# Kernel optimization log

Measured on AMD Instinct MI355X. Metric: run time of the kernel, lower is better.

The kernel has to match this reference:

```python
import jax, jax.numpy as jnp
import numpy as np

B, S, H, HKV, D = 2, 1024, 32, 8, 128


def _rope_tables(seq_len, head_dim, base=10000.0):
    inv_freq = 1.0 / (base ** (np.arange(0, head_dim, 2, dtype=np.float32) / head_dim))
    freqs = np.arange(seq_len, dtype=np.float32)[:, None] * inv_freq[None, :]  # [S, D/2]
    emb = np.concatenate([freqs, freqs], axis=-1)  # [S, D] (Llama layout)
    return jnp.asarray(np.cos(emb)), jnp.asarray(np.sin(emb))


def setup_inputs() -> dict:
    key = jax.random.key(0)
    kq, kk, kv = jax.random.split(key, 3)
    q = jax.random.normal(kq, (B, S, H, D), dtype=jnp.float32)
    k = jax.random.normal(kk, (B, S, HKV, D), dtype=jnp.float32)
    v = jax.random.normal(kv, (B, S, HKV, D), dtype=jnp.float32)
    cos, sin = _rope_tables(S, D)
    # additive causal mask [B, 1, S, S]: 0 where allowed, large negative where masked
    causal = jnp.tril(jnp.ones((S, S), dtype=bool))
    mask = jnp.where(causal, 0.0, -1e9).astype(jnp.float32)
    attention_mask = jnp.broadcast_to(mask[None, None], (B, 1, S, S))
    softmax_scale = 1.0 / float(np.sqrt(D))
    return {
        "query_states": q, "key_states": k, "value_states": v,
        "cos": cos, "sin": sin, "attention_mask": attention_mask,
        "softmax_scale": softmax_scale,
    }


def _apply_rope(x, cos, sin):
    # x: [B, S, h, D]; cos/sin: [S, D]
    d2 = x.shape[-1] // 2
    rot = jnp.concatenate([-x[..., d2:], x[..., :d2]], axis=-1)  # rotate_half
    return x * cos[None, :, None, :] + rot * sin[None, :, None, :]


def reference(query_states, key_states, value_states, cos, sin, attention_mask, softmax_scale):
    b, s, h, d = query_states.shape
    hkv = key_states.shape[2]
    g = h // hkv  # GQA group size
    q = _apply_rope(query_states, cos, sin)
    k = _apply_rope(key_states, cos, sin)
    qg = q.reshape(b, s, hkv, g, d)
    # scores: [B, Hkv, G, Q, K]
    scores = jnp.einsum('bqhgd,bkhd->bhgqk', qg, k) * softmax_scale
    scores = scores + attention_mask[:, :, None]  # [B,1,Q,K] -> broadcast over (Hkv, G)
    p = jax.nn.softmax(scores, axis=-1)
    out = jnp.einsum('bhgqk,bkhd->bqhgd', p, value_states)
    return out.reshape(b, s, h, d)
```

## Files before the change

kernel.cpp:

```cpp
#include <hip/hip_runtime.h>

#define S_LEN 1024
#define D_DIM 128
#define NH    32
#define NKV   8
#define NB    2

typedef __bf16 bf16x8 __attribute__((ext_vector_type(8)));
typedef float  f32x4  __attribute__((ext_vector_type(4)));
typedef unsigned short u16x8 __attribute__((ext_vector_type(8)));

__device__ __forceinline__ unsigned short f2bf(float f) {
    unsigned int u = __float_as_uint(f);
    u += 0x7fffu + ((u >> 16) & 1u);
    return (unsigned short)(u >> 16);
}

__device__ __forceinline__ void gld_lds16(const unsigned short* g, unsigned short* l) {
    __builtin_amdgcn_global_load_lds(
        (const __attribute__((address_space(1))) unsigned int*)(g),
        (__attribute__((address_space(3))) unsigned int*)(l), 16, 0, 0);
}

__global__ __launch_bounds__(256) void prep_kernel(
    const float* __restrict__ q, const float* __restrict__ k,
    const float* __restrict__ v, const float* __restrict__ cosb,
    const float* __restrict__ sinb, const float* __restrict__ scale_ptr,
    unsigned short* __restrict__ Qr, unsigned short* __restrict__ Kr,
    unsigned short* __restrict__ Vt)
{
    const int bx  = blockIdx.x;
    const int tid = threadIdx.x;
    __shared__ __align__(16) unsigned short tile[64][132];
    if (bx < 16384) {
        const float sc = *scale_ptr * 1.44269504088896f;
        int gid = bx * 256 + tid;
        int row = gid >> 6;
        int j   = gid & 63;
        int h  = row & (NH - 1);
        int bs = row >> 5;
        int s  = bs & (S_LEN - 1);
        int b  = bs >> 10;
        const float* qp = q + (size_t)row * D_DIM;
        float x0 = qp[j];
        float x1 = qp[j + 64];
        float c  = cosb[s * D_DIM + j];
        float sn = sinb[s * D_DIM + j];
        size_t orow = ((size_t)(b * NH + h) * S_LEN + s) * D_DIM;
        Qr[orow + j]      = f2bf((x0 * c - x1 * sn) * sc);
        Qr[orow + j + 64] = f2bf((x1 * c + x0 * sn) * sc);
    } else if (bx < 20480) {
        int gid = (bx - 16384) * 256 + tid;
        int row = gid >> 6;
        int j   = gid & 63;
        int hk = row & (NKV - 1);
        int bs = row >> 3;
        int s  = bs & (S_LEN - 1);
        int b  = bs >> 10;
        const float* kp = k + (size_t)row * D_DIM;
        float x0 = kp[j];
        float x1 = kp[j + 64];
        float c  = cosb[s * D_DIM + j];
        float sn = sinb[s * D_DIM + j];
        size_t orow = ((size_t)(b * NKV + hk) * S_LEN + s) * D_DIM;
        Kr[orow + j]      = f2bf(x0 * c - x1 * sn);
        Kr[orow + j + 64] = f2bf(x1 * c + x0 * sn);
    } else {
        int blk   = bx - 20480;
        int stile = blk & 15;
        int hk    = (blk >> 4) & (NKV - 1);
        int b     = blk >> 7;
#pragma unroll
        for (int i = 0; i < 8; i++) {
            int e    = i * 256 + tid;
            int srow = e >> 5;
            int dq   = (e & 31) * 4;
            const float* vp = v + (((size_t)(b * S_LEN + stile * 64 + srow) * NKV + hk) * D_DIM + dq);
            float4 val = *(const float4*)vp;
            tile[srow][dq + 0] = f2bf(val.x);
            tile[srow][dq + 1] = f2bf(val.y);
            tile[srow][dq + 2] = f2bf(val.z);
            tile[srow][dq + 3] = f2bf(val.w);
        }
        __syncthreads();
        size_t head = (size_t)(b * NKV + hk) * D_DIM * S_LEN;
#pragma unroll
        for (int i = 0; i < 4; i++) {
            int g  = i * 256 + tid;
            int d  = g >> 3;
            int c8 = g & 7;
            int s0 = c8 * 8;
            u16x8 pk;
#pragma unroll
            for (int jj = 0; jj < 8; jj++) pk[jj] = tile[s0 + jj][d];
            *(u16x8*)(Vt + head + (size_t)d * S_LEN + stile * 64 + s0) = pk;
        }
    }
}

__global__ __launch_bounds__(256) void attn_kernel(
    const unsigned short* __restrict__ Qr,
    const unsigned short* __restrict__ Kr,
    const unsigned short* __restrict__ Vt,
    float* __restrict__ out)
{
    const int bid = blockIdx.x;
    const int g   = bid >> 8;
    const int m   = (bid >> 6) & 3;
    const int qt  = (g == 0) ? (15 - m) : (g == 1) ? (8 + m)
                  : (g == 2) ? (7 - m)  : m;
    const int head = bid & 63;
    const int h    = head & 31;
    const int b    = head >> 5;
    const int hk   = h >> 2;

    const int tid  = threadIdx.x;
    const int w    = tid >> 6;
    const int lane = tid & 63;
    const int lr   = lane & 15;
    const int lg   = lane >> 4;

    __shared__ __align__(16) unsigned short Kt[2][32 * 128];
    __shared__ __align__(16) unsigned short Vs[2][128 * 32];
    __shared__ __align__(16) unsigned short Pb[4][16 * 32];

    const int qw = qt * 64 + w * 16;
    const int U  = 2 * qt + 2;

    const unsigned short* khead = Kr + (size_t)(b * NKV + hk) * S_LEN * D_DIM;
    const unsigned short* vhead = Vt + (size_t)(b * NKV + hk) * D_DIM * S_LEN;

    const int krow = lane >> 4;
    const int kcc  = lane & 15;
    const int vrw  = lane >> 2;
    const int vcc  = lane & 3;

    auto stage = [&](int u, int buf) {
        const unsigned short* kt = khead + (size_t)u * 32 * D_DIM;
#pragma unroll
        for (int n = 0; n < 2; n++) {
            int row = w * 8 + n * 4 + krow;
            int cc  = kcc ^ (row & 7);
            gld_lds16(kt + (size_t)row * D_DIM + cc * 8, &Kt[buf][(w * 8 + n * 4) * 128]);
        }
        const unsigned short* vt = vhead + (size_t)u * 32;
#pragma unroll
        for (int n = 0; n < 2; n++) {
            int d  = w * 32 + n * 16 + vrw;
            int cc = vcc ^ (d & 3);
            gld_lds16(vt + (size_t)d * S_LEN + cc * 8, &Vs[buf][(w * 32 + n * 16) * 32]);
        }
    };

    const unsigned short* qbase =
        Qr + ((size_t)(b * NH + h) * S_LEN + qw + lr) * D_DIM;
    bf16x8 qf[4];
#pragma unroll
    for (int kk = 0; kk < 4; kk++)
        qf[kk] = *(const bf16x8*)(qbase + lg * 8 + kk * 32);

    f32x4 o[8];
#pragma unroll
    for (int dt = 0; dt < 8; dt++) o[dt] = f32x4{0.f, 0.f, 0.f, 0.f};
    float m_run = -1e30f, lsum = 0.f;

    stage(0, 0);

#pragma unroll 1
    for (int u = 0; u < U; ++u) {
        const int cur = u & 1;
        __syncthreads();
        if (u + 1 < U) stage(u + 1, cur ^ 1);

        if (32 * u <= qw + 15) {
            const bool act1 = (32 * u + 16 <= qw + 15);

            f32x4 st[2];
            st[0] = f32x4{0.f, 0.f, 0.f, 0.f};
            st[1] = f32x4{0.f, 0.f, 0.f, 0.f};
            __builtin_amdgcn_s_setprio(1);
#pragma unroll
            for (int kj = 0; kj < 2; kj++) {
                if (kj == 0 || act1) {
                    int row = kj * 16 + lr;
#pragma unroll
                    for (int kk = 0; kk < 4; kk++) {
                        int cs = (lg + kk * 4) ^ (row & 7);
                        bf16x8 kf = *(const bf16x8*)(&Kt[cur][row * 128 + cs * 8]);
                        st[kj] = __builtin_amdgcn_mfma_f32_16x16x32_bf16(kf, qf[kk], st[kj], 0, 0, 0);
                    }
                }
            }
            __builtin_amdgcn_s_setprio(0);

            if (32 * u + 31 > qw) {
#pragma unroll
                for (int kj = 0; kj < 2; kj++)
#pragma unroll
                    for (int r = 0; r < 4; r++)
                        if (32 * u + kj * 16 + lg * 4 + r > qw + lr) st[kj][r] = -1e30f;
            }

            float mx = fmaxf(fmaxf(st[0][0], st[0][1]), fmaxf(st[0][2], st[0][3]));
            mx = fmaxf(mx, fmaxf(fmaxf(st[1][0], st[1][1]), fmaxf(st[1][2], st[1][3])));
            float pm = fmaxf(mx, __shfl_xor(mx, 16));
            pm = fmaxf(pm, __shfl_xor(pm, 32));

            if (__any(pm > m_run + 8.f)) {
                float mnew = fmaxf(m_run, pm);
                float ps   = exp2f(m_run - mnew);
                m_run = mnew;
                lsum *= ps;
#pragma unroll
                for (int r = 0; r < 4; r++) {
                    float psr = __shfl(ps, lg * 4 + r);
#pragma unroll
                    for (int dt = 0; dt < 8; dt++) o[dt][r] *= psr;
                }
            }
            float ls = 0.f;
#pragma unroll
            for (int kj = 0; kj < 2; kj++)
#pragma unroll
                for (int r = 0; r < 4; r++) {
                    float p = exp2f(st[kj][r] - m_run);
                    st[kj][r] = p;
                    ls += p;
                }
            float t = ls + __shfl_xor(ls, 16);
            t += __shfl_xor(t, 32);
            lsum += t;

            char* pw = (char*)&Pb[w][0];
#pragma unroll
            for (int kj = 0; kj < 2; kj++) {
                unsigned int w0 = (unsigned)f2bf(st[kj][0]) | ((unsigned)f2bf(st[kj][1]) << 16);
                unsigned int w1 = (unsigned)f2bf(st[kj][2]) | ((unsigned)f2bf(st[kj][3]) << 16);
                int C = (2 * kj + (lg >> 1)) ^ (lr & 3);
                *(uint2*)(pw + lr * 64 + C * 16 + (lg & 1) * 8) = uint2{w0, w1};
            }

            __builtin_amdgcn_s_setprio(1);
            int Cp = lg ^ (lr & 3);
            bf16x8 pf = *(const bf16x8*)(pw + lr * 64 + Cp * 16);
#pragma unroll
            for (int dt = 0; dt < 8; dt++) {
                int vrow = dt * 16 + lr;
                int cs2 = lg ^ (vrow & 3);
                bf16x8 vf = *(const bf16x8*)(&Vs[cur][vrow * 32 + cs2 * 8]);
                o[dt] = __builtin_amdgcn_mfma_f32_16x16x32_bf16(pf, vf, o[dt], 0, 0, 0);
            }
            __builtin_amdgcn_s_setprio(0);
        }
    }

    float rcp = 1.0f / lsum;
    float invr[4];
#pragma unroll
    for (int r = 0; r < 4; r++) invr[r] = __shfl(rcp, lg * 4 + r);
    float* obase = out + ((size_t)(b * S_LEN + qw) * NH + h) * D_DIM;
#pragma unroll
    for (int dt = 0; dt < 8; dt++)
#pragma unroll
        for (int r = 0; r < 4; r++)
            obase[(size_t)(lg * 4 + r) * NH * D_DIM + dt * 16 + lr] = o[dt][r] * invr[r];
}

extern "C" void kernel_launch(void* const* d_in, const int* in_sizes, int n_in,
                              void* d_out, int out_size, void* d_ws, size_t ws_size,
                              hipStream_t stream) {
    const float* q    = (const float*)d_in[0];
    const float* k    = (const float*)d_in[1];
    const float* v    = (const float*)d_in[2];
    const float* cosb = (const float*)d_in[3];
    const float* sinb = (const float*)d_in[4];
    const float* scale = (const float*)d_in[6];
    float* out = (float*)d_out;

    unsigned short* Qr = (unsigned short*)d_ws;
    unsigned short* Kr = Qr + (size_t)NB * NH  * S_LEN * D_DIM;
    unsigned short* Vt = Kr + (size_t)NB * NKV * S_LEN * D_DIM;

    prep_kernel<<<20736, 256, 0, stream>>>(q, k, v, cosb, sinb, scale, Qr, Kr, Vt);
    attn_kernel<<<1024, 256, 0, stream>>>(Qr, Kr, Vt, out);
}
```

Before: 73.45 us.

## Use 64-key tiles, pair causal query tiles per block, keep P in registers

The attention kernel now stages 64-key K/V tiles instead of 32 and launches 512 blocks. Each block handles two query tiles (15-p and p) in sequence, which balances causal work across blocks. The softmax probabilities are packed straight into MFMA A-operand registers, and the V fragments are gathered with split 8-byte LDS reads, so the per-wave P round trip through shared memory is gone. The costs are doubled LDS footprint, fewer blocks in flight, more registers, and a sync between the two passes.

```diff
diff --git a/kernel.cpp b/kernel.cpp
--- a/kernel.cpp
+++ b/kernel.cpp
@@ -9,6 +9,7 @@
 typedef __bf16 bf16x8 __attribute__((ext_vector_type(8)));
 typedef float  f32x4  __attribute__((ext_vector_type(4)));
 typedef unsigned short u16x8 __attribute__((ext_vector_type(8)));
+typedef unsigned int   u32x4 __attribute__((ext_vector_type(4)));
 
 __device__ __forceinline__ unsigned short f2bf(float f) {
     unsigned int u = __float_as_uint(f);
@@ -104,84 +105,79 @@
     const unsigned short* __restrict__ Vt,
     float* __restrict__ out)
 {
-    const int bid = blockIdx.x;
-    const int g   = bid >> 8;
-    const int m   = (bid >> 6) & 3;
-    const int qt  = (g == 0) ? (15 - m) : (g == 1) ? (8 + m)
-                  : (g == 2) ? (7 - m)  : m;
-    const int head = bid & 63;
-    const int h    = head & 31;
-    const int b    = head >> 5;
+    const int p    = blockIdx.x;
+    const int h    = blockIdx.y;
+    const int b    = blockIdx.z;
     const int hk   = h >> 2;
-
     const int tid  = threadIdx.x;
     const int w    = tid >> 6;
     const int lane = tid & 63;
     const int lr   = lane & 15;
     const int lg   = lane >> 4;
 
-    __shared__ __align__(16) unsigned short Kt[2][32 * 128];
-    __shared__ __align__(16) unsigned short Vs[2][128 * 32];
-    __shared__ __align__(16) unsigned short Pb[4][16 * 32];
-
-    const int qw = qt * 64 + w * 16;
-    const int U  = 2 * qt + 2;
+    __shared__ __align__(16) unsigned short Kt[2][64 * 128];
+    __shared__ __align__(16) unsigned short Vs[2][128 * 64];
 
     const unsigned short* khead = Kr + (size_t)(b * NKV + hk) * S_LEN * D_DIM;
     const unsigned short* vhead = Vt + (size_t)(b * NKV + hk) * D_DIM * S_LEN;
 
     const int krow = lane >> 4;
     const int kcc  = lane & 15;
-    const int vrw  = lane >> 2;
-    const int vcc  = lane & 3;
+    const int vrw  = lane >> 3;
+    const int vcc  = lane & 7;
 
     auto stage = [&](int u, int buf) {
-        const unsigned short* kt = khead + (size_t)u * 32 * D_DIM;
-#pragma unroll
-        for (int n = 0; n < 2; n++) {
-            int row = w * 8 + n * 4 + krow;
+        const unsigned short* kt = khead + (size_t)u * 64 * D_DIM;
+#pragma unroll
+        for (int n = 0; n < 4; n++) {
+            int row = w * 16 + n * 4 + krow;
             int cc  = kcc ^ (row & 7);
-            gld_lds16(kt + (size_t)row * D_DIM + cc * 8, &Kt[buf][(w * 8 + n * 4) * 128]);
-        }
-        const unsigned short* vt = vhead + (size_t)u * 32;
-#pragma unroll
-        for (int n = 0; n < 2; n++) {
-            int d  = w * 32 + n * 16 + vrw;
-            int cc = vcc ^ (d & 3);
-            gld_lds16(vt + (size_t)d * S_LEN + cc * 8, &Vs[buf][(w * 32 + n * 16) * 32]);
+            gld_lds16(kt + (size_t)row * D_DIM + cc * 8, &Kt[buf][(w * 16 + n * 4) * 128]);
+        }
+        const unsigned short* vt = vhead + (size_t)u * 64;
+#pragma unroll
+        for (int n = 0; n < 4; n++) {
+            int d  = w * 32 + n * 8 + vrw;
+            int cc = vcc ^ (d & 7);
+            gld_lds16(vt + (size_t)d * S_LEN + cc * 8, &Vs[buf][(w * 32 + n * 8) * 64]);
         }
     };
 
-    const unsigned short* qbase =
-        Qr + ((size_t)(b * NH + h) * S_LEN + qw + lr) * D_DIM;
-    bf16x8 qf[4];
-#pragma unroll
-    for (int kk = 0; kk < 4; kk++)
-        qf[kk] = *(const bf16x8*)(qbase + lg * 8 + kk * 32);
-
-    f32x4 o[8];
-#pragma unroll
-    for (int dt = 0; dt < 8; dt++) o[dt] = f32x4{0.f, 0.f, 0.f, 0.f};
-    float m_run = -1e30f, lsum = 0.f;
-
-    stage(0, 0);
-
 #pragma unroll 1
-    for (int u = 0; u < U; ++u) {
-        const int cur = u & 1;
-        __syncthreads();
-        if (u + 1 < U) stage(u + 1, cur ^ 1);
-
-        if (32 * u <= qw + 15) {
-            const bool act1 = (32 * u + 16 <= qw + 15);
-
-            f32x4 st[2];
-            st[0] = f32x4{0.f, 0.f, 0.f, 0.f};
-            st[1] = f32x4{0.f, 0.f, 0.f, 0.f};
+    for (int pass = 0; pass < 2; ++pass) {
+        const int qt = (pass == 0) ? (15 - p) : p;
+        const int qw = qt * 64 + w * 16;
+
+        const unsigned short* qbase =
+            Qr + ((size_t)(b * NH + h) * S_LEN + qw + lr) * D_DIM;
+        bf16x8 qf[4];
+#pragma unroll
+        for (int kk = 0; kk < 4; kk++)
+            qf[kk] = *(const bf16x8*)(qbase + lg * 8 + kk * 32);
+
+        f32x4 o[8];
+#pragma unroll
+        for (int dt = 0; dt < 8; dt++) o[dt] = f32x4{0.f, 0.f, 0.f, 0.f};
+        float m_run = -1e30f, lsum = 0.f;
+
+        if (pass) __syncthreads();
+        stage(0, 0);
+
+#pragma unroll 1
+        for (int u = 0; u <= qt; ++u) {
+            const int cur = u & 1;
+            __syncthreads();
+            if (u < qt) stage(u + 1, cur ^ 1);
+
+            const bool diag = (u == qt);
+
+            f32x4 st[4];
+#pragma unroll
+            for (int kj = 0; kj < 4; kj++) st[kj] = f32x4{0.f, 0.f, 0.f, 0.f};
             __builtin_amdgcn_s_setprio(1);
 #pragma unroll
-            for (int kj = 0; kj < 2; kj++) {
-                if (kj == 0 || act1) {
+            for (int kj = 0; kj < 4; kj++) {
+                if (!diag || kj <= w) {
                     int row = kj * 16 + lr;
 #pragma unroll
                     for (int kk = 0; kk < 4; kk++) {
@@ -193,16 +189,21 @@
             }
             __builtin_amdgcn_s_setprio(0);
 
-            if (32 * u + 31 > qw) {
-#pragma unroll
-                for (int kj = 0; kj < 2; kj++)
-#pragma unroll
-                    for (int r = 0; r < 4; r++)
-                        if (32 * u + kj * 16 + lg * 4 + r > qw + lr) st[kj][r] = -1e30f;
-            }
-
-            float mx = fmaxf(fmaxf(st[0][0], st[0][1]), fmaxf(st[0][2], st[0][3]));
-            mx = fmaxf(mx, fmaxf(fmaxf(st[1][0], st[1][1]), fmaxf(st[1][2], st[1][3])));
+            if (diag) {
+#pragma unroll
+                for (int kj = 0; kj < 4; kj++)
+                    if (kj <= w)
+#pragma unroll
+                        for (int r = 0; r < 4; r++)
+                            if (kj * 16 + lg * 4 + r > w * 16 + lr) st[kj][r] = -1e30f;
+            }
+
+            float mx = -1e30f;
+#pragma unroll
+            for (int kj = 0; kj < 4; kj++)
+                if (!diag || kj <= w)
+#pragma unroll
+                    for (int r = 0; r < 4; r++) mx = fmaxf(mx, st[kj][r]);
             float pm = fmaxf(mx, __shfl_xor(mx, 16));
             pm = fmaxf(pm, __shfl_xor(pm, 32));
 
@@ -220,50 +221,57 @@
             }
             float ls = 0.f;
 #pragma unroll
-            for (int kj = 0; kj < 2; kj++)
-#pragma unroll
-                for (int r = 0; r < 4; r++) {
-                    float p = exp2f(st[kj][r] - m_run);
-                    st[kj][r] = p;
-                    ls += p;
-                }
+            for (int kj = 0; kj < 4; kj++)
+                if (!diag || kj <= w)
+#pragma unroll
+                    for (int r = 0; r < 4; r++) {
+                        float pv = exp2f(st[kj][r] - m_run);
+                        st[kj][r] = pv;
+                        ls += pv;
+                    }
             float t = ls + __shfl_xor(ls, 16);
             t += __shfl_xor(t, 32);
             lsum += t;
 
-            char* pw = (char*)&Pb[w][0];
-#pragma unroll
-            for (int kj = 0; kj < 2; kj++) {
-                unsigned int w0 = (unsigned)f2bf(st[kj][0]) | ((unsigned)f2bf(st[kj][1]) << 16);
-                unsigned int w1 = (unsigned)f2bf(st[kj][2]) | ((unsigned)f2bf(st[kj][3]) << 16);
-                int C = (2 * kj + (lg >> 1)) ^ (lr & 3);
-                *(uint2*)(pw + lr * 64 + C * 16 + (lg & 1) * 8) = uint2{w0, w1};
-            }
-
+            const char* vbase = (const char*)&Vs[cur][0];
+            const int x = lr & 7;
             __builtin_amdgcn_s_setprio(1);
-            int Cp = lg ^ (lr & 3);
-            bf16x8 pf = *(const bf16x8*)(pw + lr * 64 + Cp * 16);
-#pragma unroll
-            for (int dt = 0; dt < 8; dt++) {
-                int vrow = dt * 16 + lr;
-                int cs2 = lg ^ (vrow & 3);
-                bf16x8 vf = *(const bf16x8*)(&Vs[cur][vrow * 32 + cs2 * 8]);
-                o[dt] = __builtin_amdgcn_mfma_f32_16x16x32_bf16(pf, vf, o[dt], 0, 0, 0);
+#pragma unroll
+            for (int kk2 = 0; kk2 < 2; kk2++) {
+                if (!diag || w >= 2 * kk2) {
+                    unsigned int d0 = (unsigned)f2bf(st[2 * kk2][0])     | ((unsigned)f2bf(st[2 * kk2][1]) << 16);
+                    unsigned int d1 = (unsigned)f2bf(st[2 * kk2][2])     | ((unsigned)f2bf(st[2 * kk2][3]) << 16);
+                    unsigned int d2 = (unsigned)f2bf(st[2 * kk2 + 1][0]) | ((unsigned)f2bf(st[2 * kk2 + 1][1]) << 16);
+                    unsigned int d3 = (unsigned)f2bf(st[2 * kk2 + 1][2]) | ((unsigned)f2bf(st[2 * kk2 + 1][3]) << 16);
+                    u32x4 paw = {d0, d1, d2, d3};
+                    bf16x8 pa = __builtin_bit_cast(bf16x8, paw);
+                    const int c16 = 4 * kk2 + (lg >> 1);
+                    const int sub = (lg & 1) * 8;
+#pragma unroll
+                    for (int dt = 0; dt < 8; dt++) {
+                        const char* vrow = vbase + (dt * 16 + lr) * 128;
+                        uint2 vlo = *(const uint2*)(vrow + ((c16       ^ x) << 4) + sub);
+                        uint2 vhi = *(const uint2*)(vrow + (((c16 + 2) ^ x) << 4) + sub);
+                        u32x4 vw = {vlo.x, vlo.y, vhi.x, vhi.y};
+                        bf16x8 vf = __builtin_bit_cast(bf16x8, vw);
+                        o[dt] = __builtin_amdgcn_mfma_f32_16x16x32_bf16(pa, vf, o[dt], 0, 0, 0);
+                    }
+                }
             }
             __builtin_amdgcn_s_setprio(0);
         }
+
+        float rcp = 1.0f / lsum;
+        float invr[4];
+#pragma unroll
+        for (int r = 0; r < 4; r++) invr[r] = __shfl(rcp, lg * 4 + r);
+        float* obase = out + ((size_t)(b * S_LEN + qw) * NH + h) * D_DIM;
+#pragma unroll
+        for (int dt = 0; dt < 8; dt++)
+#pragma unroll
+            for (int r = 0; r < 4; r++)
+                obase[(size_t)(lg * 4 + r) * NH * D_DIM + dt * 16 + lr] = o[dt][r] * invr[r];
     }
-
-    float rcp = 1.0f / lsum;
-    float invr[4];
-#pragma unroll
-    for (int r = 0; r < 4; r++) invr[r] = __shfl(rcp, lg * 4 + r);
-    float* obase = out + ((size_t)(b * S_LEN + qw) * NH + h) * D_DIM;
-#pragma unroll
-    for (int dt = 0; dt < 8; dt++)
-#pragma unroll
-        for (int r = 0; r < 4; r++)
-            obase[(size_t)(lg * 4 + r) * NH * D_DIM + dt * 16 + lr] = o[dt][r] * invr[r];
 }
 
 extern "C" void kernel_launch(void* const* d_in, const int* in_sizes, int n_in,
@@ -282,5 +290,6 @@
     unsigned short* Vt = Kr + (size_t)NB * NKV * S_LEN * D_DIM;
 
     prep_kernel<<<20736, 256, 0, stream>>>(q, k, v, cosb, sinb, scale, Qr, Kr, Vt);
-    attn_kernel<<<1024, 256, 0, stream>>>(Qr, Kr, Vt, out);
-}
+    dim3 grid(8, NH, NB);
+    attn_kernel<<<grid, 256, 0, stream>>>(Qr, Kr, Vt, out);
+}
```

Result: faster. 68.34 us (-7.0%).
